# Kernel tuning notes

Hardware: AMD Instinct MI355X
Metric: run time of the kernel (lower is better)

Reference implementation:

```python
import jax, jax.numpy as jnp
import numpy as np

EMB, HEADS, T_BLK = 1024, 16, 2048
B, T = 2, 2048
HD = EMB // HEADS


def setup_inputs() -> dict:
    key = jax.random.key(0)
    ks = jax.random.split(key, 9)
    s = 1.0 / np.sqrt(EMB)
    return {
        "x": jax.random.normal(ks[0], (B, T, EMB), jnp.float32),
        "Wq": jax.random.normal(ks[1], (EMB, EMB), jnp.float32) * s,
        "bq": jax.random.normal(ks[2], (EMB,), jnp.float32) * s,
        "Wk": jax.random.normal(ks[3], (EMB, EMB), jnp.float32) * s,
        "bk": jax.random.normal(ks[4], (EMB,), jnp.float32) * s,
        "Wv": jax.random.normal(ks[5], (EMB, EMB), jnp.float32) * s,
        "bv": jax.random.normal(ks[6], (EMB,), jnp.float32) * s,
        "Wo": jax.random.normal(ks[7], (EMB, EMB), jnp.float32) * s,
        "bo": jax.random.normal(ks[8], (EMB,), jnp.float32) * s,
    }


def reference(x, Wq, bq, Wk, bk, Wv, bv, Wo, bo):
    # eval mode: dropout is identity
    Bn, Tn, C = x.shape
    def proj(W, b):
        y = x @ W.T + b                      # [B,T,C]
        return y.reshape(Bn, Tn, HEADS, HD).transpose(0, 2, 1, 3)  # [B,H,T,hd]
    q, k, v = proj(Wq, bq), proj(Wk, bk), proj(Wv, bv)
    scores = jnp.einsum('bhqd,bhkd->bhqk', q, k) * (HD ** -0.5)  # [B,H,T,T]
    causal = jnp.tril(jnp.ones((Tn, Tn), dtype=bool))
    scores = jnp.where(causal, scores, -jnp.inf)
    w = jax.nn.softmax(scores, axis=-1)
    out = jnp.einsum('bhqk,bhkd->bhqd', w, v)                    # [B,H,T,hd]
    out = out.transpose(0, 2, 1, 3).reshape(Bn, Tn, C)
    return out @ Wo.T + bo
```

## Files before the change

kernel.cpp:

```cpp
#include <hip/hip_runtime.h>
#include <stdint.h>

#define EMB   1024
#define HEADS 16
#define HD    64
#define BB    2
#define TT    2048
#define MTOT  (BB*TT)
#define LDA   72
#define LDP   72

#define ELX (4194304u)
#define ELW (1048576u)

#define CSCALE (0.125f * 1.44269504088896f)

typedef __attribute__((ext_vector_type(8))) short short8;
typedef __attribute__((ext_vector_type(4))) float f32x4;
typedef __attribute__((ext_vector_type(4))) unsigned short us4;

__device__ __forceinline__ float bf2f(ushort u) {
  union { uint32_t u; float f; } x; x.u = ((uint32_t)u) << 16; return x.f;
}
__device__ __forceinline__ ushort f2bf(float f) {
  union { float f; uint32_t u; } x; x.f = f;
  uint32_t u = x.u;
  u += 0x7fffu + ((u >> 16) & 1u);
  return (ushort)(u >> 16);
}
__device__ __forceinline__ uint32_t pack2(uint32_t lo, uint32_t hi) {
  return (lo >> 16) | (hi & 0xFFFF0000u);
}
__device__ __forceinline__ short8 pack8(f32x4 a, f32x4 b) {
  union { f32x4 v; uint32_t u[4]; } A, B;
  A.v = a; B.v = b;
  union { uint32_t d[4]; short8 s; } R;
  R.d[0] = pack2(A.u[0], A.u[1]);
  R.d[1] = pack2(A.u[2], A.u[3]);
  R.d[2] = pack2(B.u[0], B.u[1]);
  R.d[3] = pack2(B.u[2], B.u[3]);
  return R.s;
}
__device__ __forceinline__ short8 cvt8_rne(const float* f) {
  f32x4 a = *(const f32x4*)f;
  f32x4 b = *(const f32x4*)(f + 4);
  short8 r;
  r[0] = (short)f2bf(a[0]); r[1] = (short)f2bf(a[1]);
  r[2] = (short)f2bf(a[2]); r[3] = (short)f2bf(a[3]);
  r[4] = (short)f2bf(b[0]); r[5] = (short)f2bf(b[1]);
  r[6] = (short)f2bf(b[2]); r[7] = (short)f2bf(b[3]);
  return r;
}

__device__ __forceinline__ void gll16(const void* g, void* l) {
  __builtin_amdgcn_global_load_lds((const __attribute__((address_space(1))) void*)g,
                                   (__attribute__((address_space(3))) void*)l,
                                   16, 0, 0);
}

__global__ void detect_dtype(const uint32_t* __restrict__ x, int* __restrict__ flag) {
  const int lane = threadIdx.x & 63;
  int cnt = 0;
#pragma unroll
  for (int i = 0; i < 4; ++i) {
    const uint32_t v = x[lane * 4 + i];
    const uint32_t e = ((v & 0xFFFFu) >> 7) & 0xFFu;
    cnt += (e >= 0x70u && e <= 0x8Fu) ? 1 : 0;
  }
#pragma unroll
  for (int off = 1; off < 64; off <<= 1) cnt += __shfl_xor(cnt, off);
  if (lane == 0) *flag = (cnt > 128) ? 1 : 0;
}

__global__ __launch_bounds__(256) void convert3(const void* __restrict__ w0,
                                                const void* __restrict__ w1,
                                                const void* __restrict__ w2,
                                                ushort* __restrict__ dst,
                                                const int* __restrict__ flag) {
  const size_t i = ((size_t)blockIdx.x * 256 + threadIdx.x) * 8;
  const int wi = (int)(i >> 20);
  const size_t off = i & (ELW - 1);
  const void* src = (wi == 0) ? w0 : (wi == 1) ? w1 : w2;
  if (*flag) *(short8*)(dst + i) = *(const short8*)((const ushort*)src + off);
  else       *(short8*)(dst + i) = cvt8_rne((const float*)src + off);
}

template<bool ABF>
__device__ __forceinline__ void qkv_core(const void* __restrict__ xp,
                                         const ushort* __restrict__ W,
                                         int m0, int n0r,
                                         ushort* As, ushort* Bs,
                                         f32x4 acc[4][4]) {
  const int tid  = threadIdx.x;
  const int w    = tid >> 6;
  const int lane = tid & 63;
  const int quad = lane >> 4;
  const int l16  = lane & 15;
  const int wr   = w >> 1, wc = w & 1;

  const int srow = tid >> 3;
  const int scol = (tid & 7) ^ (srow & 7);
  const size_t aoff = (size_t)(m0 + srow) * EMB + scol * 8;
  const size_t boff = (size_t)(n0r + srow) * EMB + scol * 8;

  f32x4 ar[8];
  if constexpr (!ABF) {
    const float* xf = (const float*)xp;
#pragma unroll
    for (int j = 0; j < 4; ++j) {
      ar[2 * j]     = *(const f32x4*)(xf + aoff + (size_t)j * 32 * EMB);
      ar[2 * j + 1] = *(const f32x4*)(xf + aoff + (size_t)j * 32 * EMB + 4);
    }
  }

  const int rsw = l16 & 7;

  for (int it = 0; it < 16; ++it) {
    const int k0 = it * 64;
    __syncthreads();
    if constexpr (ABF) {
      const ushort* xu = (const ushort*)xp;
#pragma unroll
      for (int j = 0; j < 4; ++j)
        gll16(xu + aoff + (size_t)j * 32 * EMB + k0, As + j * 2048 + w * 512);
    } else {
#pragma unroll
      for (int j = 0; j < 4; ++j)
        *(short8*)&As[((size_t)j * 256 + tid) * 8] = pack8(ar[2 * j], ar[2 * j + 1]);
    }
#pragma unroll
    for (int j = 0; j < 4; ++j)
      gll16(W + boff + (size_t)j * 32 * EMB + k0, Bs + j * 2048 + w * 512);
    if constexpr (!ABF) {
      if (it + 1 < 16) {
        const float* xf = (const float*)xp;
#pragma unroll
        for (int j = 0; j < 4; ++j) {
          ar[2 * j]     = *(const f32x4*)(xf + aoff + (size_t)j * 32 * EMB + k0 + 64);
          ar[2 * j + 1] = *(const f32x4*)(xf + aoff + (size_t)j * 32 * EMB + k0 + 68);
        }
      }
    }
    __syncthreads();

#pragma unroll
    for (int ks = 0; ks < 2; ++ks) {
      const int pc = (ks * 4 + quad) ^ rsw;
      short8 a_[4], b_[4];
#pragma unroll
      for (int mi = 0; mi < 4; ++mi)
        a_[mi] = *(const short8*)&As[(wr * 64 + mi * 16 + l16) * 64 + pc * 8];
#pragma unroll
      for (int ni = 0; ni < 4; ++ni)
        b_[ni] = *(const short8*)&Bs[(wc * 64 + ni * 16 + l16) * 64 + pc * 8];
#pragma unroll
      for (int mi = 0; mi < 4; ++mi)
#pragma unroll
        for (int ni = 0; ni < 4; ++ni)
          acc[mi][ni] = __builtin_amdgcn_mfma_f32_16x16x32_bf16(a_[mi], b_[ni], acc[mi][ni], 0, 0, 0);
    }
  }
}

__global__ __launch_bounds__(256) void qkv_pipe(const void* __restrict__ x,
                                                const ushort* __restrict__ w3,
                                                const void* __restrict__ bq,
                                                const void* __restrict__ bk,
                                                const void* __restrict__ bv,
                                                ushort* __restrict__ qo,
                                                ushort* __restrict__ ko,
                                                ushort* __restrict__ vo,
                                                const int* __restrict__ flag) {
  __shared__ __align__(16) ushort As[128 * 64];
  __shared__ __align__(16) ushort Bs[128 * 64];
  const int bid = blockIdx.x;
  const int xcd = bid & 7;
  const int i   = bid >> 3;
  const int nt  = xcd * 3 + (i % 3);
  const int mt  = i / 3;
  const int mat = nt >> 3;
  const int n0r = (nt & 7) * 128;
  const int m0  = mt * 128;
  const ushort* W  = w3 + (size_t)mat * ELW;
  const void* bias = (mat == 0) ? bq : (mat == 1) ? bk : bv;

  f32x4 acc[4][4];
#pragma unroll
  for (int a = 0; a < 4; ++a)
#pragma unroll
    for (int b = 0; b < 4; ++b) acc[a][b] = (f32x4){0.f, 0.f, 0.f, 0.f};

  const int isbf = *flag;
  if (isbf) qkv_core<true >(x, W, m0, n0r, As, Bs, acc);
  else      qkv_core<false>(x, W, m0, n0r, As, Bs, acc);

  const int tid  = threadIdx.x;
  const int w    = tid >> 6;
  const int lane = tid & 63;
  const int quad = lane >> 4;
  const int l16  = lane & 15;
  const int wr   = w >> 1, wc = w & 1;
  ushort* dst = (mat == 0) ? qo : ko;
  const float sc = (mat == 0) ? CSCALE : 1.0f;

#pragma unroll
  for (int ni = 0; ni < 4; ++ni) {
    const int n = n0r + wc * 64 + ni * 16 + l16;
    const float bv_ = isbf ? bf2f(((const ushort*)bias)[n]) : ((const float*)bias)[n];
    const int h = n >> 6, d = n & 63;
#pragma unroll
    for (int mi = 0; mi < 4; ++mi) {
      const int mbase = m0 + wr * 64 + mi * 16 + quad * 4;
      const int b = mbase >> 11, t = mbase & (TT - 1);
      if (mat == 2) {
        us4 pk;
#pragma unroll
        for (int r = 0; r < 4; ++r) pk[r] = f2bf(acc[mi][ni][r] + bv_);
        *(us4*)&vo[((size_t)((b * HEADS + h) * HD + d)) * TT + t] = pk;
      } else {
#pragma unroll
        for (int r = 0; r < 4; ++r)
          dst[((size_t)((b * HEADS + h) * TT + t + r)) * HD + d] = f2bf((acc[mi][ni][r] + bv_) * sc);
      }
    }
  }
}

__global__ __launch_bounds__(256) void attn3(const ushort* __restrict__ qw,
                                             const ushort* __restrict__ kw,
                                             const ushort* __restrict__ vtw,
                                             ushort* __restrict__ out) {
  __shared__ __align__(16) ushort Ks[64 * LDA];
  __shared__ __align__(16) ushort Vts[64 * LDA];
  __shared__ __align__(16) ushort Ps[4][16 * LDA];

  const int bid = blockIdx.x;
  const int j  = bid >> 8;
  const int r8 = bid & 255;
  const int qh = r8 & 31;
  const int bh = j * 8 + (r8 >> 5);
  int qt;
  if      (j == 0) qt = qh;
  else if (j == 1) qt = 31 - qh;
  else if (j == 2) qt = (qh + 16) & 31;
  else             qt = 31 - ((qh + 16) & 31);
  const int h = bh & (HEADS - 1);
  const int b = bh >> 4;

  const int tid  = threadIdx.x;
  const int w    = tid >> 6;
  const int lane = tid & 63;
  const int quad = lane >> 4;
  const int l16  = lane & 15;

  const size_t hoff = ((size_t)(b * HEADS + h)) * TT * HD;
  const ushort* Qg = qw + hoff;
  const ushort* Kg = kw + hoff;
  const ushort* Vg = vtw + hoff;
  const int q0 = qt * 64;

  short8 qf[2];
  {
    const ushort* qrow = Qg + (size_t)(q0 + w * 16 + l16) * HD;
    qf[0] = *(const short8*)(qrow + quad * 8);
    qf[1] = *(const short8*)(qrow + 32 + quad * 8);
  }

  const int row = tid >> 2;
  const int c0  = (tid & 3) * 16;
  const ushort* Kbase = Kg + (size_t)row * HD + c0;
  const ushort* Vbase = Vg + (size_t)row * TT + c0;

  float lsp[4] = {0.f, 0.f, 0.f, 0.f};
  f32x4 O[4];
#pragma unroll
  for (int ni = 0; ni < 4; ++ni) O[ni] = (f32x4){0.f, 0.f, 0.f, 0.f};

  auto compute_tile = [&](int kt) {
    f32x4 s[4];
#pragma unroll
    for (int ni = 0; ni < 4; ++ni) s[ni] = (f32x4){0.f, 0.f, 0.f, 0.f};
#pragma unroll
    for (int ks = 0; ks < 2; ++ks) {
#pragma unroll
      for (int ni = 0; ni < 4; ++ni) {
        short8 kb = *(const short8*)&Ks[(ni * 16 + l16) * LDA + ks * 32 + quad * 8];
        s[ni] = __builtin_amdgcn_mfma_f32_16x16x32_bf16(kb, qf[ks], s[ni], 0, 0, 0);
      }
    }
    if (kt == qt) {
      const int qq = w * 16 + l16;
#pragma unroll
      for (int ni = 0; ni < 4; ++ni) {
#pragma unroll
        for (int r = 0; r < 4; ++r)
          if (ni * 16 + quad * 4 + r > qq) s[ni][r] = -__builtin_inff();
      }
    }
#pragma unroll
    for (int ni = 0; ni < 4; ++ni) {
      union { float f; uint32_t u; } p0, p1, p2, p3;
      p0.f = exp2f(s[ni][0]); p1.f = exp2f(s[ni][1]);
      p2.f = exp2f(s[ni][2]); p3.f = exp2f(s[ni][3]);
      lsp[ni] += (p0.f + p1.f) + (p2.f + p3.f);
      uint2 dw;
      dw.x = pack2(p0.u, p1.u);
      dw.y = pack2(p2.u, p3.u);
      *(uint2*)&Ps[w][l16 * LDA + ni * 16 + quad * 4] = dw;
    }
#pragma unroll
    for (int ks = 0; ks < 2; ++ks) {
      short8 a = *(const short8*)&Ps[w][l16 * LDA + ks * 32 + quad * 8];
#pragma unroll
      for (int ni = 0; ni < 4; ++ni) {
        short8 vb = *(const short8*)&Vts[(ni * 16 + l16) * LDA + ks * 32 + quad * 8];
        O[ni] = __builtin_amdgcn_mfma_f32_16x16x32_bf16(a, vb, O[ni], 0, 0, 0);
      }
    }
  };

  short8 ak0, ak1, av0, av1;
  short8 bk0, bk1, bv0, bv1;
  ak0 = *(const short8*)(Kbase);
  ak1 = *(const short8*)(Kbase + 8);
  av0 = *(const short8*)(Vbase);
  av1 = *(const short8*)(Vbase + 8);

  for (int kt = 0; kt <= qt; ) {
    __syncthreads();
    *(short8*)&Ks[row * LDA + c0]      = ak0;
    *(short8*)&Ks[row * LDA + c0 + 8]  = ak1;
    *(short8*)&Vts[row * LDA + c0]     = av0;
    *(short8*)&Vts[row * LDA + c0 + 8] = av1;
    if (kt + 1 <= qt) {
      const size_t ko_ = (size_t)(kt + 1) * 64 * HD;
      bk0 = *(const short8*)(Kbase + ko_);
      bk1 = *(const short8*)(Kbase + ko_ + 8);
      bv0 = *(const short8*)(Vbase + (kt + 1) * 64);
      bv1 = *(const short8*)(Vbase + (kt + 1) * 64 + 8);
    }
    __syncthreads();
    compute_tile(kt);
    ++kt;
    if (kt > qt) break;

    __syncthreads();
    *(short8*)&Ks[row * LDA + c0]      = bk0;
    *(short8*)&Ks[row * LDA + c0 + 8]  = bk1;
    *(short8*)&Vts[row * LDA + c0]     = bv0;
    *(short8*)&Vts[row * LDA + c0 + 8] = bv1;
    if (kt + 1 <= qt) {
      const size_t ko_ = (size_t)(kt + 1) * 64 * HD;
      ak0 = *(const short8*)(Kbase + ko_);
      ak1 = *(const short8*)(Kbase + ko_ + 8);
      av0 = *(const short8*)(Vbase + (kt + 1) * 64);
      av1 = *(const short8*)(Vbase + (kt + 1) * 64 + 8);
    }
    __syncthreads();
    compute_tile(kt);
    ++kt;
  }

  float lst = (lsp[0] + lsp[1]) + (lsp[2] + lsp[3]);
  lst += __shfl_xor(lst, 16);
  lst += __shfl_xor(lst, 32);

#pragma unroll
  for (int r = 0; r < 4; ++r) {
    const float inv = 1.0f / __shfl(lst, (lane & 48) | (quad * 4 + r));
    const int t = q0 + w * 16 + quad * 4 + r;
#pragma unroll
    for (int ni = 0; ni < 4; ++ni) {
      out[((size_t)(b * TT + t)) * EMB + h * HD + ni * 16 + l16] = f2bf(O[ni][r] * inv);
    }
  }
}

template<bool WBF>
__device__ __forceinline__ void proj_core(const ushort* __restrict__ A,
                                          const void* __restrict__ Wo,
                                          int m0, int n0,
                                          ushort* As, ushort* Ws,
                                          f32x4 acc[2][4]) {
  const int tid  = threadIdx.x;
  const int w    = tid >> 6;
  const int lane = tid & 63;
  const int quad = lane >> 4;
  const int l16  = lane & 15;
  const int arow = tid >> 1;
  const int acol = (tid & 1) * 32;
  const int brow = tid >> 2;
  const int bcol = (tid & 3) * 16;

  const size_t aoff = (size_t)(m0 + arow) * EMB + acol;
  const size_t boff = (size_t)(n0 + brow) * EMB + bcol;

  short8 ab[3][4];
  short8 wb[3][2];
  f32x4  wf[3][4];

#pragma unroll
  for (int s = 0; s < 2; ++s) {
#pragma unroll
    for (int i = 0; i < 4; ++i)
      ab[s][i] = *(const short8*)(A + aoff + 64 * s + 8 * i);
    if constexpr (WBF) {
      wb[s][0] = *(const short8*)((const ushort*)Wo + boff + 64 * s);
      wb[s][1] = *(const short8*)((const ushort*)Wo + boff + 64 * s + 8);
    } else {
#pragma unroll
      for (int i = 0; i < 4; ++i)
        wf[s][i] = *(const f32x4*)((const float*)Wo + boff + 64 * s + 4 * i);
    }
  }

#pragma unroll
  for (int it = 0; it < 16; ++it) {
    const int k0 = it * 64;
    const int cur = it % 3, nxt = (it + 2) % 3;
    __syncthreads();
#pragma unroll
    for (int i = 0; i < 4; ++i)
      *(short8*)&As[arow * LDP + acol + 8 * i] = ab[cur][i];
    if constexpr (WBF) {
      *(short8*)&Ws[brow * LDP + bcol]     = wb[cur][0];
      *(short8*)&Ws[brow * LDP + bcol + 8] = wb[cur][1];
    } else {
      *(short8*)&Ws[brow * LDP + bcol]     = pack8(wf[cur][0], wf[cur][1]);
      *(short8*)&Ws[brow * LDP + bcol + 8] = pack8(wf[cur][2], wf[cur][3]);
    }
    if (it + 2 < 16) {
      const int kn = k0 + 128;
#pragma unroll
      for (int i = 0; i < 4; ++i)
        ab[nxt][i] = *(const short8*)(A + aoff + kn + 8 * i);
      if constexpr (WBF) {
        wb[nxt][0] = *(const short8*)((const ushort*)Wo + boff + kn);
        wb[nxt][1] = *(const short8*)((const ushort*)Wo + boff + kn + 8);
      } else {
#pragma unroll
        for (int i = 0; i < 4; ++i)
          wf[nxt][i] = *(const f32x4*)((const float*)Wo + boff + kn + 4 * i);
      }
    }
    __syncthreads();

#pragma unroll
    for (int ks = 0; ks < 2; ++ks) {
      short8 a_[2], b_[4];
#pragma unroll
      for (int i = 0; i < 2; ++i)
        a_[i] = *(const short8*)&As[(w * 32 + i * 16 + l16) * LDP + ks * 32 + quad * 8];
#pragma unroll
      for (int i = 0; i < 4; ++i)
        b_[i] = *(const short8*)&Ws[(i * 16 + l16) * LDP + ks * 32 + quad * 8];
#pragma unroll
      for (int mi = 0; mi < 2; ++mi)
#pragma unroll
        for (int ni = 0; ni < 4; ++ni)
          acc[mi][ni] = __builtin_amdgcn_mfma_f32_16x16x32_bf16(a_[mi], b_[ni], acc[mi][ni], 0, 0, 0);
    }
  }
}

__global__ __launch_bounds__(256) void proj_pipe(const ushort* __restrict__ A,
                                                 const void* __restrict__ Wo,
                                                 const void* __restrict__ bo,
                                                 void* __restrict__ out,
                                                 const int* __restrict__ flag) {
  __shared__ __align__(16) ushort As[128 * LDP];
  __shared__ __align__(16) ushort Ws[64 * LDP];
  const int nt = blockIdx.x & 15;
  const int mt = blockIdx.x >> 4;
  const int n0 = nt * 64;
  const int m0 = mt * 128;

  f32x4 acc[2][4];
#pragma unroll
  for (int i = 0; i < 2; ++i)
#pragma unroll
    for (int jj = 0; jj < 4; ++jj) acc[i][jj] = (f32x4){0.f, 0.f, 0.f, 0.f};

  const int isbf = *flag;
  if (isbf) proj_core<true >(A, Wo, m0, n0, As, Ws, acc);
  else      proj_core<false>(A, Wo, m0, n0, As, Ws, acc);

  const int tid  = threadIdx.x;
  const int w    = tid >> 6;
  const int lane = tid & 63;
  const int quad = lane >> 4;
  const int l16  = lane & 15;

#pragma unroll
  for (int ni = 0; ni < 4; ++ni) {
    const int n = n0 + ni * 16 + l16;
    const float bv_ = isbf ? bf2f(((const ushort*)bo)[n]) : ((const float*)bo)[n];
#pragma unroll
    for (int mi = 0; mi < 2; ++mi) {
#pragma unroll
      for (int r = 0; r < 4; ++r) {
        const int m = m0 + w * 32 + mi * 16 + quad * 4 + r;
        const float v = acc[mi][ni][r] + bv_;
        if (isbf) ((ushort*)out)[(size_t)m * EMB + n] = f2bf(v);
        else      ((float*) out)[(size_t)m * EMB + n] = v;
      }
    }
  }
}

extern "C" void kernel_launch(void* const* d_in, const int* in_sizes, int n_in,
                              void* d_out, int out_size, void* d_ws, size_t ws_size,
                              hipStream_t stream) {
  const void* x  = d_in[0];
  const void* Wq = d_in[1];
  const void* bq = d_in[2];
  const void* Wk = d_in[3];
  const void* bk = d_in[4];
  const void* Wv = d_in[5];
  const void* bv = d_in[6];
  const void* Wo = d_in[7];
  const void* bo = d_in[8];

  int* flag = (int*)d_ws;
  ushort* base = (ushort*)((char*)d_ws + 256);

  ushort* q_ws  = base;
  ushort* k_ws  = q_ws + ELX;
  ushort* vt_ws = k_ws + ELX;
  ushort* w3    = vt_ws + ELX;
  ushort* o_ws  = vt_ws + ELX;

  detect_dtype<<<dim3(1), dim3(64), 0, stream>>>((const uint32_t*)x, flag);
  convert3<<<dim3(1536), dim3(256), 0, stream>>>(Wq, Wk, Wv, w3, flag);
  qkv_pipe<<<dim3(768), dim3(256), 0, stream>>>(x, w3, bq, bk, bv,
                                                q_ws, k_ws, vt_ws, flag);
  attn3<<<dim3(1024), dim3(256), 0, stream>>>(q_ws, k_ws, vt_ws, o_ws);
  proj_pipe<<<dim3(512), dim3(256), 0, stream>>>(o_ws, Wo, bo, d_out, flag);
}
```

Baseline: 217.3 us.

## Enlarge QKV GEMM tiles to 256x192 with double-buffered LDS pipeline

The QKV projection kernel moves from 128x128 tiles with 4 waves to 256x192 tiles with 8 waves (512 threads) and double-buffered shared memory. The next K-slice is prefetched while MFMAs run on the current one, which removes one barrier per iteration. The N tile now spans the concatenated Q/K/V weights, so the matrix index is chosen per column. The aim is higher arithmetic intensity and latency hiding, at the cost of 256 blocks instead of 768, so fewer blocks than CUs, plus much more LDS and register pressure.

```diff
diff --git a/kernel.cpp b/kernel.cpp
--- a/kernel.cpp
+++ b/kernel.cpp
@@ -85,142 +85,155 @@
   else       *(short8*)(dst + i) = cvt8_rne((const float*)src + off);
 }
 
+#define ASZ (256 * 64)
+#define BSZ (192 * 64)
+
 template<bool ABF>
 __device__ __forceinline__ void qkv_core(const void* __restrict__ xp,
                                          const ushort* __restrict__ W,
                                          int m0, int n0r,
-                                         ushort* As, ushort* Bs,
-                                         f32x4 acc[4][4]) {
+                                         ushort* As0, ushort* Bs0,
+                                         f32x4 acc[8][3]) {
   const int tid  = threadIdx.x;
   const int w    = tid >> 6;
   const int lane = tid & 63;
   const int quad = lane >> 4;
   const int l16  = lane & 15;
-  const int wr   = w >> 1, wc = w & 1;
-
-  const int srow = tid >> 3;
-  const int scol = (tid & 7) ^ (srow & 7);
-  const size_t aoff = (size_t)(m0 + srow) * EMB + scol * 8;
-  const size_t boff = (size_t)(n0r + srow) * EMB + scol * 8;
+  const int wr   = w >> 2, wc = w & 3;
+
+  const int prow = tid >> 3;
+  const int c    = tid & 7;
+  const int sw   = c ^ (prow & 7);
+  const int rsw  = l16 & 7;
+
+  const ushort* xu = (const ushort*)xp;
+  const float*  xf = (const float*)xp;
 
   f32x4 ar[8];
-  if constexpr (!ABF) {
-    const float* xf = (const float*)xp;
-#pragma unroll
-    for (int j = 0; j < 4; ++j) {
-      ar[2 * j]     = *(const f32x4*)(xf + aoff + (size_t)j * 32 * EMB);
-      ar[2 * j + 1] = *(const f32x4*)(xf + aoff + (size_t)j * 32 * EMB + 4);
-    }
-  }
-
-  const int rsw = l16 & 7;
-
-  for (int it = 0; it < 16; ++it) {
-    const int k0 = it * 64;
-    __syncthreads();
-    if constexpr (ABF) {
-      const ushort* xu = (const ushort*)xp;
-#pragma unroll
-      for (int j = 0; j < 4; ++j)
-        gll16(xu + aoff + (size_t)j * 32 * EMB + k0, As + j * 2048 + w * 512);
-    } else {
-#pragma unroll
-      for (int j = 0; j < 4; ++j)
-        *(short8*)&As[((size_t)j * 256 + tid) * 8] = pack8(ar[2 * j], ar[2 * j + 1]);
-    }
-#pragma unroll
-    for (int j = 0; j < 4; ++j)
-      gll16(W + boff + (size_t)j * 32 * EMB + k0, Bs + j * 2048 + w * 512);
-    if constexpr (!ABF) {
-      if (it + 1 < 16) {
-        const float* xf = (const float*)xp;
-#pragma unroll
-        for (int j = 0; j < 4; ++j) {
-          ar[2 * j]     = *(const f32x4*)(xf + aoff + (size_t)j * 32 * EMB + k0 + 64);
-          ar[2 * j + 1] = *(const f32x4*)(xf + aoff + (size_t)j * 32 * EMB + k0 + 68);
-        }
-      }
-    }
-    __syncthreads();
-
-#pragma unroll
-    for (int ks = 0; ks < 2; ++ks) {
-      const int pc = (ks * 4 + quad) ^ rsw;
-      short8 a_[4], b_[4];
-#pragma unroll
-      for (int mi = 0; mi < 4; ++mi)
-        a_[mi] = *(const short8*)&As[(wr * 64 + mi * 16 + l16) * 64 + pc * 8];
-#pragma unroll
-      for (int ni = 0; ni < 4; ++ni)
-        b_[ni] = *(const short8*)&Bs[(wc * 64 + ni * 16 + l16) * 64 + pc * 8];
-#pragma unroll
-      for (int mi = 0; mi < 4; ++mi)
-#pragma unroll
-        for (int ni = 0; ni < 4; ++ni)
-          acc[mi][ni] = __builtin_amdgcn_mfma_f32_16x16x32_bf16(a_[mi], b_[ni], acc[mi][ni], 0, 0, 0);
-    }
-  }
-}
-
-__global__ __launch_bounds__(256) void qkv_pipe(const void* __restrict__ x,
-                                                const ushort* __restrict__ w3,
-                                                const void* __restrict__ bq,
-                                                const void* __restrict__ bk,
-                                                const void* __restrict__ bv,
-                                                ushort* __restrict__ qo,
-                                                ushort* __restrict__ ko,
-                                                ushort* __restrict__ vo,
-                                                const int* __restrict__ flag) {
-  __shared__ __align__(16) ushort As[128 * 64];
-  __shared__ __align__(16) ushort Bs[128 * 64];
+
+  auto stageB = [&](int cur, int kt) {
+#pragma unroll
+    for (int g = 0; g < 3; ++g)
+      gll16(W + (size_t)(n0r + g * 64 + prow) * EMB + kt * 64 + sw * 8,
+            Bs0 + cur * BSZ + g * 4096 + w * 512);
+  };
+  auto stageA_gll = [&](int cur, int kt) {
+#pragma unroll
+    for (int g = 0; g < 4; ++g)
+      gll16(xu + (size_t)(m0 + g * 64 + prow) * EMB + kt * 64 + sw * 8,
+            As0 + cur * ASZ + g * 4096 + w * 512);
+  };
+  auto stageA_issue = [&](int kt) {
+#pragma unroll
+    for (int g = 0; g < 4; ++g) {
+      const float* src = xf + (size_t)(m0 + g * 64 + prow) * EMB + kt * 64 + c * 8;
+      ar[2 * g]     = *(const f32x4*)(src);
+      ar[2 * g + 1] = *(const f32x4*)(src + 4);
+    }
+  };
+  auto stageA_write = [&](int cur) {
+#pragma unroll
+    for (int g = 0; g < 4; ++g)
+      *(short8*)&As0[cur * ASZ + (g * 64 + prow) * 64 + sw * 8] =
+          pack8(ar[2 * g], ar[2 * g + 1]);
+  };
+
+  stageB(0, 0);
+  if constexpr (ABF) stageA_gll(0, 0);
+  else { stageA_issue(0); stageA_write(0); }
+  __syncthreads();
+
+  for (int t = 0; t < 16; ++t) {
+    const int cur = t & 1, nxt = cur ^ 1;
+    if (t < 15) {
+      stageB(nxt, t + 1);
+      if constexpr (ABF) stageA_gll(nxt, t + 1);
+      else stageA_issue(t + 1);
+    }
+
+    const ushort* Ab = As0 + cur * ASZ;
+    const ushort* Bb = Bs0 + cur * BSZ;
+    short8 bf_[3][2];
+#pragma unroll
+    for (int ni = 0; ni < 3; ++ni)
+#pragma unroll
+      for (int ks = 0; ks < 2; ++ks)
+        bf_[ni][ks] = *(const short8*)&Bb[(wc * 48 + ni * 16 + l16) * 64 +
+                                          ((ks * 4 + quad) ^ rsw) * 8];
+#pragma unroll
+    for (int mi = 0; mi < 8; ++mi) {
+      const int arow = (wr * 128 + mi * 16 + l16) * 64;
+      short8 a0 = *(const short8*)&Ab[arow + ((quad) ^ rsw) * 8];
+      short8 a1 = *(const short8*)&Ab[arow + ((4 + quad) ^ rsw) * 8];
+#pragma unroll
+      for (int ni = 0; ni < 3; ++ni) {
+        acc[mi][ni] = __builtin_amdgcn_mfma_f32_16x16x32_bf16(a0, bf_[ni][0], acc[mi][ni], 0, 0, 0);
+        acc[mi][ni] = __builtin_amdgcn_mfma_f32_16x16x32_bf16(a1, bf_[ni][1], acc[mi][ni], 0, 0, 0);
+      }
+    }
+    if (t < 15) { if constexpr (!ABF) stageA_write(nxt); }
+    __syncthreads();
+  }
+}
+
+__global__ __launch_bounds__(512, 2) void qkv_pipe(const void* __restrict__ x,
+                                                   const ushort* __restrict__ w3,
+                                                   const void* __restrict__ bq,
+                                                   const void* __restrict__ bk,
+                                                   const void* __restrict__ bv,
+                                                   ushort* __restrict__ qo,
+                                                   ushort* __restrict__ ko,
+                                                   ushort* __restrict__ vo,
+                                                   const int* __restrict__ flag) {
+  __shared__ __align__(16) ushort As2[2 * ASZ];
+  __shared__ __align__(16) ushort Bs2[2 * BSZ];
   const int bid = blockIdx.x;
-  const int xcd = bid & 7;
-  const int i   = bid >> 3;
-  const int nt  = xcd * 3 + (i % 3);
-  const int mt  = i / 3;
-  const int mat = nt >> 3;
-  const int n0r = (nt & 7) * 128;
-  const int m0  = mt * 128;
-  const ushort* W  = w3 + (size_t)mat * ELW;
-  const void* bias = (mat == 0) ? bq : (mat == 1) ? bk : bv;
-
-  f32x4 acc[4][4];
-#pragma unroll
-  for (int a = 0; a < 4; ++a)
-#pragma unroll
-    for (int b = 0; b < 4; ++b) acc[a][b] = (f32x4){0.f, 0.f, 0.f, 0.f};
+  const int u   = bid & 15;
+  const int mt  = bid >> 4;
+  const int nt  = (u & 7) * 2 + (u >> 3);
+  const int m0  = mt * 256;
+  const int n0r = nt * 192;
+
+  f32x4 acc[8][3];
+#pragma unroll
+  for (int a = 0; a < 8; ++a)
+#pragma unroll
+    for (int b = 0; b < 3; ++b) acc[a][b] = (f32x4){0.f, 0.f, 0.f, 0.f};
 
   const int isbf = *flag;
-  if (isbf) qkv_core<true >(x, W, m0, n0r, As, Bs, acc);
-  else      qkv_core<false>(x, W, m0, n0r, As, Bs, acc);
+  if (isbf) qkv_core<true >(x, w3, m0, n0r, As2, Bs2, acc);
+  else      qkv_core<false>(x, w3, m0, n0r, As2, Bs2, acc);
 
   const int tid  = threadIdx.x;
   const int w    = tid >> 6;
   const int lane = tid & 63;
   const int quad = lane >> 4;
   const int l16  = lane & 15;
-  const int wr   = w >> 1, wc = w & 1;
-  ushort* dst = (mat == 0) ? qo : ko;
-  const float sc = (mat == 0) ? CSCALE : 1.0f;
-
-#pragma unroll
-  for (int ni = 0; ni < 4; ++ni) {
-    const int n = n0r + wc * 64 + ni * 16 + l16;
-    const float bv_ = isbf ? bf2f(((const ushort*)bias)[n]) : ((const float*)bias)[n];
-    const int h = n >> 6, d = n & 63;
-#pragma unroll
-    for (int mi = 0; mi < 4; ++mi) {
-      const int mbase = m0 + wr * 64 + mi * 16 + quad * 4;
-      const int b = mbase >> 11, t = mbase & (TT - 1);
+  const int wr   = w >> 2, wc = w & 3;
+
+#pragma unroll
+  for (int ni = 0; ni < 3; ++ni) {
+    const int n   = n0r + wc * 48 + ni * 16 + l16;
+    const int mat = n >> 10, nn = n & 1023;
+    const void* bias = (mat == 0) ? bq : (mat == 1) ? bk : bv;
+    const float bv_ = isbf ? bf2f(((const ushort*)bias)[nn]) : ((const float*)bias)[nn];
+    const int h = nn >> 6, d = nn & 63;
+    const float sc = (mat == 0) ? CSCALE : 1.0f;
+    ushort* dqk = (mat == 0) ? qo : ko;
+#pragma unroll
+    for (int mi = 0; mi < 8; ++mi) {
+      const int m = m0 + wr * 128 + mi * 16 + quad * 4;
+      const int b = m >> 11, tt = m & (TT - 1);
       if (mat == 2) {
         us4 pk;
 #pragma unroll
         for (int r = 0; r < 4; ++r) pk[r] = f2bf(acc[mi][ni][r] + bv_);
-        *(us4*)&vo[((size_t)((b * HEADS + h) * HD + d)) * TT + t] = pk;
+        *(us4*)&vo[((size_t)((b * HEADS + h) * HD + d)) * TT + tt] = pk;
       } else {
 #pragma unroll
         for (int r = 0; r < 4; ++r)
-          dst[((size_t)((b * HEADS + h) * TT + t + r)) * HD + d] = f2bf((acc[mi][ni][r] + bv_) * sc);
+          dqk[((size_t)((b * HEADS + h) * TT + tt + r)) * HD + d] =
+              f2bf((acc[mi][ni][r] + bv_) * sc);
       }
     }
   }
@@ -532,7 +545,7 @@
 
   detect_dtype<<<dim3(1), dim3(64), 0, stream>>>((const uint32_t*)x, flag);
   convert3<<<dim3(1536), dim3(256), 0, stream>>>(Wq, Wk, Wv, w3, flag);
-  qkv_pipe<<<dim3(768), dim3(256), 0, stream>>>(x, w3, bq, bk, bv,
+  qkv_pipe<<<dim3(256), dim3(512), 0, stream>>>(x, w3, bq, bk, bv,
                                                 q_ws, k_ws, vt_ws, flag);
   attn3<<<dim3(1024), dim3(256), 0, stream>>>(q_ws, k_ws, vt_ws, o_ws);
   proj_pipe<<<dim3(512), dim3(256), 0, stream>>>(o_ws, Wo, bo, d_out, flag);
```

Result: no change. 215.1 us (-1.0%).
